# Optimization experiments

Measured on AMD Instinct MI355X. Metric: run time of the kernel, lower is better.

Reference implementation:

```python
import jax, jax.numpy as jnp
import numpy as np

F = 256       # in_src/in_dst feature dim (feat_dict)
HID = 256     # hidden_dim
K = 16        # sampled neighbors per dst node (fixed fan-out)
N_REVIEW = 16384
N_USER = 65536
N_PRODUCT = 65536
EPS = 1e-5


def setup_inputs() -> dict:
    key = jax.random.key(0)
    ks = jax.random.split(key, 24)
    rn = lambda k, shape, s=0.05: jax.random.normal(k, shape, jnp.float32) * s
    inp = {
        'x_user': jax.random.normal(ks[0], (N_USER, F), jnp.float32),
        'x_product': jax.random.normal(ks[1], (N_PRODUCT, F), jnp.float32),
        'x_review': jax.random.normal(ks[2], (N_REVIEW, F), jnp.float32),
        'nbr_user': jax.random.randint(ks[3], (N_REVIEW, K), 0, N_USER),
        'nbr_product': jax.random.randint(ks[4], (N_REVIEW, K), 0, N_PRODUCT),
    }
    i = 5
    for pre in ('u_', 'p_'):
        inp[pre + 'Wih'] = rn(ks[i], (4 * F, F)); i += 1      # LSTM input weights (gates i,f,g,o)
        inp[pre + 'Whh'] = rn(ks[i], (4 * F, F)); i += 1      # LSTM hidden weights
        inp[pre + 'bih'] = jnp.zeros((4 * F,), jnp.float32)
        inp[pre + 'bhh'] = jnp.zeros((4 * F,), jnp.float32)
        inp[pre + 'Wself'] = rn(ks[i], (HID, F)); i += 1      # SAGEConv fc_self
        inp[pre + 'Wneigh'] = rn(ks[i], (HID, F)); i += 1     # SAGEConv fc_neigh
        inp[pre + 'bconv'] = jnp.zeros((HID,), jnp.float32)   # SAGEConv bias
    inp['ln_g'] = jnp.ones((HID,), jnp.float32)
    inp['ln_b'] = jnp.zeros((HID,), jnp.float32)
    inp['bn_g'] = jnp.ones((HID,), jnp.float32)
    inp['bn_b'] = jnp.zeros((HID,), jnp.float32)
    inp['W1'] = rn(ks[i], (HID, HID)); i += 1
    inp['b1'] = jnp.zeros((HID,), jnp.float32)
    inp['W2'] = rn(ks[i], (2, HID)); i += 1
    inp['b2'] = jnp.zeros((2,), jnp.float32)
    return inp


def _lstm_last(x, Wih, Whh, bih, bhh):
    # x: [N, K, F] neighbor sequences; returns final hidden state [N, F]
    n, _, f = x.shape
    b = bih + bhh
    def step(carry, xt):  # xt: [N, F]
        h, c = carry
        gates = xt @ Wih.T + h @ Whh.T + b  # [N, 4F]
        ig, fg, gg, og = jnp.split(gates, 4, axis=-1)
        c = jax.nn.sigmoid(fg) * c + jax.nn.sigmoid(ig) * jnp.tanh(gg)
        h = jax.nn.sigmoid(og) * jnp.tanh(c)
        return (h, c), None
    h0 = jnp.zeros((n, f), x.dtype)
    (h, _), _ = jax.lax.scan(step, (h0, h0), jnp.swapaxes(x, 0, 1))
    return h


def _sage_rel(x_src, x_dst, nbr, Wih, Whh, bih, bhh, Wself, Wneigh, bconv):
    # gather neighbor features [N_dst, K, F] (feat_drop is identity at eval)
    nb = x_src[nbr]
    h_neigh = _lstm_last(nb, Wih, Whh, bih, bhh)            # [N_dst, F]
    rst = x_dst @ Wself.T + h_neigh @ Wneigh.T + bconv       # [N_dst, HID]
    return jax.nn.gelu(rst, approximate=False)               # activation=nn.GELU()


def reference(x_user, x_product, x_review, nbr_user, nbr_product,
              u_Wih, u_Whh, u_bih, u_bhh, u_Wself, u_Wneigh, u_bconv,
              p_Wih, p_Whh, p_bih, p_bhh, p_Wself, p_Wneigh, p_bconv,
              ln_g, ln_b, bn_g, bn_b, W1, b1, W2, b2):
    # HeteroGraphConv(aggregate='sum') over the two relations into 'review'
    h = (_sage_rel(x_user, x_review, nbr_user, u_Wih, u_Whh, u_bih, u_bhh,
                   u_Wself, u_Wneigh, u_bconv)
         + _sage_rel(x_product, x_review, nbr_product, p_Wih, p_Whh, p_bih, p_bhh,
                     p_Wself, p_Wneigh, p_bconv))
    # LayerNorm
    mu = jnp.mean(h, axis=-1, keepdims=True)
    var = jnp.var(h, axis=-1, keepdims=True)
    h = (h - mu) * jax.lax.rsqrt(var + EPS) * ln_g + ln_b
    # clf head: Dropout (identity at eval) -> BatchNorm1d (batch stats) -> MLP
    bm = jnp.mean(h, axis=0, keepdims=True)
    bv = jnp.var(h, axis=0, keepdims=True)
    h = (h - bm) * jax.lax.rsqrt(bv + EPS) * bn_g + bn_b
    h = jax.nn.gelu(h @ W1.T + b1, approximate=False)
    return h @ W2.T + b2  # [N_REVIEW, 2]
```

## Files before the change

kernel.cpp:

```cpp
#include <hip/hip_runtime.h>
#include <math.h>

#define NREV 16384
#define NUSER 65536
#define NPROD 65536
#define KNBR 16
#define LDK 72

typedef __attribute__((ext_vector_type(8))) short short8;
typedef __attribute__((ext_vector_type(4))) float f32x4;
typedef unsigned short u16;

__device__ __forceinline__ u16 f2bf(float f){
  union { float f; unsigned u; } x; x.f = f;
  unsigned r = x.u + 0x7fffu + ((x.u >> 16) & 1u);
  return (u16)(r >> 16);
}
__device__ __forceinline__ float bf2f(u16 u){
  union { unsigned u; float f; } x; x.u = ((unsigned)u) << 16;
  return x.f;
}
__device__ __forceinline__ float fexp2(float x){ return __builtin_amdgcn_exp2f(x); }
__device__ __forceinline__ float frcp(float x){ return __builtin_amdgcn_rcpf(x); }
#define LOG2E 1.4426950408889634f
__device__ __forceinline__ float sigf(float x){ return frcp(1.f + fexp2(-LOG2E*x)); }
__device__ __forceinline__ float tanh_fast(float x){ return 1.f - 2.f*frcp(1.f + fexp2(2.f*LOG2E*x)); }
__device__ __forceinline__ float gelu_fast(float x){
  float u = 0.7978845608f*x*(1.f + 0.044715f*x*x);
  return 0.5f*x*(1.f + tanh_fast(u));
}

__global__ void cvt_kernel(const float* __restrict__ src, u16* __restrict__ dst, int n4){
  int i = blockIdx.x*256 + threadIdx.x;
  if(i < n4){
    float4 v = reinterpret_cast<const float4*>(src)[i];
    ushort4 o; o.x=f2bf(v.x); o.y=f2bf(v.y); o.z=f2bf(v.z); o.w=f2bf(v.w);
    reinterpret_cast<ushort4*>(dst)[i] = o;
  }
}

__global__ void pack_lstm_kernel(const float* __restrict__ Wihp, const float* __restrict__ Whhp,
                                 const float* __restrict__ bihp, const float* __restrict__ bhhp,
                                 u16* __restrict__ Bpp, float* __restrict__ bpp){
  int n = blockIdx.x;
  int g = n & 3, j = n >> 2;
  int m = g*256 + j;
  int k = threadIdx.x;
  Bpp[(size_t)n*512 + k]       = f2bf(Wihp[(size_t)m*256 + k]);
  Bpp[(size_t)n*512 + 256 + k] = f2bf(Whhp[(size_t)m*256 + k]);
  if(k == 0) bpp[n] = bihp[m] + bhhp[m];
}

__global__ void pack_sage_kernel(const float* __restrict__ Wselfp, const float* __restrict__ Wneighp,
                                 u16* __restrict__ Bsp){
  int n = blockIdx.x;
  int k = threadIdx.x;
  Bsp[(size_t)n*512 + k]       = f2bf(Wselfp[(size_t)n*256 + k]);
  Bsp[(size_t)n*512 + 256 + k] = f2bf(Wneighp[(size_t)n*256 + k]);
}

__global__ __launch_bounds__(256, 4) void xw_kernel(
    const float* __restrict__ x, const u16* __restrict__ Bp,
    const float* __restrict__ bp, u16* __restrict__ xwout)
{
  __shared__ u16 sA[128*LDK];
  __shared__ u16 sB[128*LDK];
  int tid = threadIdx.x;
  int p = blockIdx.x;
  int xcd = p & 7, g = p >> 3;
  int nt = g & 7;
  int rt = (g >> 3) * 8 + xcd;
  f32x4 acc[4][4];
  #pragma unroll
  for(int i=0;i<4;++i)
    #pragma unroll
    for(int j=0;j<4;++j) acc[i][j] = (f32x4){0.f,0.f,0.f,0.f};
  int lane = tid & 63, w = tid >> 6, wr = w >> 1, wc = w & 1;
  int ci = tid & 7, r0 = tid >> 3;
  int rrow = lane & 15, lhi = lane >> 4, kb = lhi * 8;

  for(int kt=0; kt<4; ++kt){
    __syncthreads();
    #pragma unroll
    for(int pp=0; pp<4; ++pp){
      int row = pp*32 + r0;
      const float* srcA = x + (size_t)(rt*128 + row)*256 + kt*64 + ci*8;
      float4 a0 = *(const float4*)srcA;
      float4 a1 = *(const float4*)(srcA + 4);
      short8 s;
      s[0]=f2bf(a0.x); s[1]=f2bf(a0.y); s[2]=f2bf(a0.z); s[3]=f2bf(a0.w);
      s[4]=f2bf(a1.x); s[5]=f2bf(a1.y); s[6]=f2bf(a1.z); s[7]=f2bf(a1.w);
      *(short8*)&sA[row*LDK + ci*8] = s;
      *(short8*)&sB[row*LDK + ci*8] =
        *(const short8*)(Bp + (size_t)(nt*128 + row)*512 + kt*64 + ci*8);
    }
    __syncthreads();
    #pragma unroll
    for(int kk=0; kk<2; ++kk){
      short8 af[4], bfv[4];
      #pragma unroll
      for(int ni=0;ni<4;++ni) af[ni]  = *(const short8*)&sB[(wc*64+ni*16+rrow)*LDK + kk*32 + kb];
      #pragma unroll
      for(int mi=0;mi<4;++mi) bfv[mi] = *(const short8*)&sA[(wr*64+mi*16+rrow)*LDK + kk*32 + kb];
      #pragma unroll
      for(int ni=0;ni<4;++ni)
        #pragma unroll
        for(int mi=0;mi<4;++mi)
          acc[ni][mi] = __builtin_amdgcn_mfma_f32_16x16x32_bf16(af[ni], bfv[mi], acc[ni][mi], 0, 0, 0);
    }
  }
  #pragma unroll
  for(int mi=0;mi<4;++mi){
    size_t node = (size_t)(rt*128 + wr*64 + mi*16 + rrow);
    u16* dst = xwout + node*1024;
    #pragma unroll
    for(int ni=0;ni<4;++ni){
      int n0 = nt*128 + wc*64 + ni*16 + lhi*4;
      float4 bv = *(const float4*)&bp[n0];
      ushort4 o;
      o.x = f2bf(acc[ni][mi][0] + bv.x);
      o.y = f2bf(acc[ni][mi][1] + bv.y);
      o.z = f2bf(acc[ni][mi][2] + bv.z);
      o.w = f2bf(acc[ni][mi][3] + bv.w);
      *(ushort4*)(dst + n0) = o;
    }
  }
}

__global__ __launch_bounds__(256, 3) void lstm_step10_kernel(
    const u16* __restrict__ xw, const int* __restrict__ nbr, int t,
    const u16* __restrict__ Bh,
    const u16* __restrict__ hin, u16* __restrict__ hout, float* __restrict__ cT)
{
  __shared__ u16 sA[128*LDK];
  __shared__ u16 sB[128*LDK];
  int tid = threadIdx.x;
  int p = blockIdx.x;
  int xcd = p & 7, g = p >> 3;
  int nt = g & 7;
  int rt = (g >> 3) * 8 + xcd;
  int lane = tid & 63, w = tid >> 6, wr = w >> 1, wc = w & 1;
  int ci = tid & 7, r0 = tid >> 3;
  int rrow = lane & 15, lhi = lane >> 4, kb = lhi * 8;

  int node[4];
  #pragma unroll
  for(int mi=0;mi<4;++mi)
    node[mi] = nbr[(size_t)(rt*128 + wr*64 + mi*16 + rrow)*KNBR + t];
  ushort4 xv[4][4];
  #pragma unroll
  for(int mi=0;mi<4;++mi)
    #pragma unroll
    for(int ni=0;ni<4;++ni){
      int n0 = nt*128 + wc*64 + ni*16 + lhi*4;
      xv[mi][ni] = *(const ushort4*)(xw + (size_t)node[mi]*1024 + n0);
    }

  f32x4 acc[4][4];
  #pragma unroll
  for(int i=0;i<4;++i)
    #pragma unroll
    for(int j=0;j<4;++j) acc[i][j] = (f32x4){0.f,0.f,0.f,0.f};

  if(t > 0){
    for(int kt=0; kt<4; ++kt){
      __syncthreads();
      #pragma unroll
      for(int pp=0; pp<4; ++pp){
        int row = pp*32 + r0;
        *(short8*)&sA[row*LDK + ci*8] =
          *(const short8*)(hin + (size_t)(rt*128 + row)*256 + kt*64 + ci*8);
        *(short8*)&sB[row*LDK + ci*8] =
          *(const short8*)(Bh + (size_t)(nt*128 + row)*512 + kt*64 + ci*8);
      }
      __syncthreads();
      #pragma unroll
      for(int kk=0; kk<2; ++kk){
        short8 af[4], bfv[4];
        #pragma unroll
        for(int ni=0;ni<4;++ni) af[ni]  = *(const short8*)&sB[(wc*64+ni*16+rrow)*LDK + kk*32 + kb];
        #pragma unroll
        for(int mi=0;mi<4;++mi) bfv[mi] = *(const short8*)&sA[(wr*64+mi*16+rrow)*LDK + kk*32 + kb];
        #pragma unroll
        for(int ni=0;ni<4;++ni)
          #pragma unroll
          for(int mi=0;mi<4;++mi)
            acc[ni][mi] = __builtin_amdgcn_mfma_f32_16x16x32_bf16(af[ni], bfv[mi], acc[ni][mi], 0, 0, 0);
      }
    }
  }

  float cv[4][4];
  #pragma unroll
  for(int mi=0;mi<4;++mi)
    #pragma unroll
    for(int ni=0;ni<4;++ni){
      cv[mi][ni] = 0.f;
      if(t > 0){
        int j = nt*32 + wc*16 + ni*4 + lhi;
        cv[mi][ni] = cT[(size_t)j*NREV + rt*128 + wr*64 + mi*16 + rrow];
      }
    }

  #pragma unroll
  for(int mi=0;mi<4;++mi){
    int rg = rt*128 + wr*64 + mi*16 + rrow;
    #pragma unroll
    for(int ni=0;ni<4;++ni){
      int j = nt*32 + wc*16 + ni*4 + lhi;
      float ig = bf2f(xv[mi][ni].x) + acc[ni][mi][0];
      float fg = bf2f(xv[mi][ni].y) + acc[ni][mi][1];
      float gg = bf2f(xv[mi][ni].z) + acc[ni][mi][2];
      float og = bf2f(xv[mi][ni].w) + acc[ni][mi][3];
      float cn = sigf(fg)*cv[mi][ni] + sigf(ig)*tanh_fast(gg);
      cT[(size_t)j*NREV + rg] = cn;
      hout[(size_t)rg*256 + j] = f2bf(sigf(og)*tanh_fast(cn));
    }
  }
}

template<int MODE>
__global__ __launch_bounds__(256) void gemm_act_kernel(
    const u16* __restrict__ A0, const u16* __restrict__ A1,
    const u16* __restrict__ Bp, const float* __restrict__ bias,
    float* __restrict__ outF, u16* __restrict__ outH)
{
  constexpr int KT   = (MODE == 2) ? 4 : 8;
  constexpr int KTOT = KT * 64;
  __shared__ u16 sA[128*LDK];
  __shared__ u16 sB[128*LDK];
  int tid = threadIdx.x;
  int rt = blockIdx.x, nt = blockIdx.y;
  f32x4 acc[4][4];
  #pragma unroll
  for(int i=0;i<4;++i)
    #pragma unroll
    for(int j=0;j<4;++j) acc[i][j] = (f32x4){0.f,0.f,0.f,0.f};
  int lane = tid & 63, w = tid >> 6, wr = w >> 1, wc = w & 1;
  int ci = tid & 7, r0 = tid >> 3;
  int rrow = lane & 15, kb = (lane >> 4) * 8;

  for(int kt=0; kt<KT; ++kt){
    __syncthreads();
    #pragma unroll
    for(int pp=0; pp<4; ++pp){
      int row = pp*32 + r0;
      const u16* srcA = (kt < 4)
        ? (A0 + ((size_t)(rt*128 + row))*256 + kt*64)
        : (A1 + ((size_t)(rt*128 + row))*256 + (kt-4)*64);
      *(short8*)&sA[row*LDK + ci*8] = *(const short8*)(srcA + ci*8);
      const u16* srcB = Bp + ((size_t)(nt*128 + row))*KTOT + kt*64;
      *(short8*)&sB[row*LDK + ci*8] = *(const short8*)(srcB + ci*8);
    }
    __syncthreads();
    #pragma unroll
    for(int kk=0; kk<2; ++kk){
      short8 af[4], bfv[4];
      #pragma unroll
      for(int mi=0;mi<4;++mi) af[mi] = *(const short8*)&sA[(wr*64+mi*16+rrow)*LDK + kk*32 + kb];
      #pragma unroll
      for(int ni=0;ni<4;++ni) bfv[ni] = *(const short8*)&sB[(wc*64+ni*16+rrow)*LDK + kk*32 + kb];
      #pragma unroll
      for(int mi=0;mi<4;++mi)
        #pragma unroll
        for(int ni=0;ni<4;++ni)
          acc[mi][ni] = __builtin_amdgcn_mfma_f32_16x16x32_bf16(af[mi], bfv[ni], acc[mi][ni], 0, 0, 0);
    }
  }
  #pragma unroll
  for(int mi=0;mi<4;++mi)
    #pragma unroll
    for(int ni=0;ni<4;++ni){
      int col  = nt*128 + wc*64 + ni*16 + rrow;
      int rowb = rt*128 + wr*64 + mi*16 + (lane>>4)*4;
      float bv = bias[col];
      #pragma unroll
      for(int q=0;q<4;++q){
        float x = acc[mi][ni][q] + bv;
        float gl = gelu_fast(x);
        size_t idx = (size_t)(rowb+q)*256 + col;
        if(MODE == 0)      outF[idx] = gl;
        else if(MODE == 1) outF[idx] += gl;
        else               outH[idx] = f2bf(gl);
      }
    }
}

__global__ void ln_kernel(const float* __restrict__ hs, const float* __restrict__ g,
                          const float* __restrict__ b, u16* __restrict__ hlnp){
  int w = threadIdx.x >> 6, lane = threadIdx.x & 63;
  int r = blockIdx.x*4 + w;
  const float* row = hs + (size_t)r*256;
  float4 v = *(const float4*)(row + lane*4);
  float s  = v.x+v.y+v.z+v.w;
  float ss = v.x*v.x + v.y*v.y + v.z*v.z + v.w*v.w;
  #pragma unroll
  for(int d=1; d<64; d<<=1){ s += __shfl_xor(s, d, 64); ss += __shfl_xor(ss, d, 64); }
  float mu  = s  * (1.f/256.f);
  float var = ss * (1.f/256.f) - mu*mu;
  float rs  = rsqrtf(var + 1e-5f);
  float4 gv = *(const float4*)(g + lane*4);
  float4 bv = *(const float4*)(b + lane*4);
  ushort4 o;
  o.x = f2bf((v.x-mu)*rs*gv.x + bv.x);
  o.y = f2bf((v.y-mu)*rs*gv.y + bv.y);
  o.z = f2bf((v.z-mu)*rs*gv.z + bv.z);
  o.w = f2bf((v.w-mu)*rs*gv.w + bv.w);
  *(ushort4*)(hlnp + (size_t)r*256 + lane*4) = o;
}

__global__ void colstats_kernel(const u16* __restrict__ hlnp, float* __restrict__ cs, float* __restrict__ cq){
  int cix = threadIdx.x;
  size_t rb = (size_t)blockIdx.x * 128;
  float s=0.f, q=0.f;
  for(int rr=0; rr<128; ++rr){
    float v = bf2f(hlnp[(rb+rr)*256 + cix]);
    s += v; q += v*v;
  }
  atomicAdd(&cs[cix], s);
  atomicAdd(&cq[cix], q);
}

__global__ void bnstat_kernel(const float* __restrict__ cs, const float* __restrict__ cq,
                              const float* __restrict__ bng, const float* __restrict__ bnb,
                              float* __restrict__ bns, float* __restrict__ bnt){
  int cix = threadIdx.x;
  float bm = cs[cix] * (1.f/16384.f);
  float bv = cq[cix] * (1.f/16384.f) - bm*bm;
  float s  = bng[cix] * rsqrtf(bv + 1e-5f);
  bns[cix] = s;
  bnt[cix] = bnb[cix] - bm*s;
}

__global__ void w1fold_kernel(const float* __restrict__ W1p, const float* __restrict__ b1p,
                              const float* __restrict__ bns, const float* __restrict__ bnt,
                              u16* __restrict__ W1fp, float* __restrict__ b1fp){
  __shared__ float red[4];
  int n = blockIdx.x, k = threadIdx.x;
  int lane = k & 63, w = k >> 6;
  float wv = W1p[(size_t)n*256 + k];
  W1fp[(size_t)n*256 + k] = f2bf(wv * bns[k]);
  float p = wv * bnt[k];
  #pragma unroll
  for(int d=1; d<64; d<<=1) p += __shfl_xor(p, d, 64);
  if(lane == 0) red[w] = p;
  __syncthreads();
  if(k == 0) b1fp[n] = b1p[n] + red[0] + red[1] + red[2] + red[3];
}

__global__ void head_kernel(const u16* __restrict__ z, const float* __restrict__ W2p,
                            const float* __restrict__ b2p, float* __restrict__ outp){
  int w = threadIdx.x >> 6, lane = threadIdx.x & 63;
  int r = blockIdx.x*4 + w;
  const u16* zr = z + (size_t)r*256;
  ushort4 v = *(const ushort4*)(zr + lane*4);
  float z0=bf2f(v.x), z1v=bf2f(v.y), z2=bf2f(v.z), z3=bf2f(v.w);
  float4 wa = *(const float4*)(W2p + lane*4);
  float4 wb = *(const float4*)(W2p + 256 + lane*4);
  float p0 = z0*wa.x + z1v*wa.y + z2*wa.z + z3*wa.w;
  float p1 = z0*wb.x + z1v*wb.y + z2*wb.z + z3*wb.w;
  #pragma unroll
  for(int d=1; d<64; d<<=1){ p0 += __shfl_xor(p0,d,64); p1 += __shfl_xor(p1,d,64); }
  if(lane == 0){
    outp[(size_t)r*2]   = p0 + b2p[0];
    outp[(size_t)r*2+1] = p1 + b2p[1];
  }
}

extern "C" void kernel_launch(void* const* d_in, const int* in_sizes, int n_in,
                              void* d_out, int out_size, void* d_ws, size_t ws_size,
                              hipStream_t stream){
  (void)in_sizes; (void)n_in; (void)out_size;
  const float* x_user    = (const float*)d_in[0];
  const float* x_product = (const float*)d_in[1];
  const float* x_review  = (const float*)d_in[2];
  const int*   nbr_user  = (const int*)d_in[3];
  const int*   nbr_prod  = (const int*)d_in[4];
  const float* Wih[2]    = {(const float*)d_in[5],  (const float*)d_in[12]};
  const float* Whh[2]    = {(const float*)d_in[6],  (const float*)d_in[13]};
  const float* bih[2]    = {(const float*)d_in[7],  (const float*)d_in[14]};
  const float* bhh[2]    = {(const float*)d_in[8],  (const float*)d_in[15]};
  const float* Wself[2]  = {(const float*)d_in[9],  (const float*)d_in[16]};
  const float* Wneigh[2] = {(const float*)d_in[10], (const float*)d_in[17]};
  const float* bconv[2]  = {(const float*)d_in[11], (const float*)d_in[18]};
  const float* ln_g=(const float*)d_in[19], *ln_b=(const float*)d_in[20];
  const float* bn_g=(const float*)d_in[21], *bn_b=(const float*)d_in[22];
  const float* W1=(const float*)d_in[23], *b1=(const float*)d_in[24];
  const float* W2=(const float*)d_in[25], *b2=(const float*)d_in[26];
  float* out = (float*)d_out;

  char* base = (char*)d_ws;
  size_t off = 0;
  auto alloc = [&](size_t bytes)->char* { char* r = base + off; off += (bytes + 255) & ~(size_t)255; return r; };
  u16*   xr   = (u16*)  alloc((size_t)NREV*256*2);
  float* hsum = (float*)alloc((size_t)NREV*256*4);
  u16*   Bp[2]; Bp[0]=(u16*)alloc(1024*512*2); Bp[1]=(u16*)alloc(1024*512*2);
  float* bp[2]; bp[0]=(float*)alloc(4096);     bp[1]=(float*)alloc(4096);
  u16*   Bs[2]; Bs[0]=(u16*)alloc(256*512*2);  Bs[1]=(u16*)alloc(256*512*2);
  float* csum = (float*)alloc(1024);
  float* csq  = (float*)alloc(1024);
  float* bns  = (float*)alloc(1024);
  float* bnt  = (float*)alloc(1024);
  u16*   W1f  = (u16*)  alloc(256*256*2);
  float* b1f  = (float*)alloc(1024);
  u16*   hA   = (u16*)  alloc((size_t)NREV*256*2);
  u16*   hB   = (u16*)  alloc((size_t)NREV*256*2);
  float* cT   = (float*)alloc((size_t)NREV*256*4);
  u16*   xW   = (u16*)  alloc((size_t)NUSER*1024*2);
  if(off > ws_size) return;
  u16* hln = hA;
  u16* z1  = hB;

  cvt_kernel<<<dim3(4096),256,0,stream>>>(x_review, xr, NREV*256/4);
  for(int rel=0; rel<2; ++rel){
    pack_lstm_kernel<<<dim3(1024),256,0,stream>>>(Wih[rel],Whh[rel],bih[rel],bhh[rel],Bp[rel],bp[rel]);
    pack_sage_kernel<<<dim3(256), 256,0,stream>>>(Wself[rel],Wneigh[rel],Bs[rel]);
  }
  hipMemsetAsync(csum, 0, 1024, stream);
  hipMemsetAsync(csq,  0, 1024, stream);

  for(int rel=0; rel<2; ++rel){
    const float* xs = rel ? x_product : x_user;
    const int*   nb = rel ? nbr_prod  : nbr_user;
    xw_kernel<<<dim3(4096),256,0,stream>>>(xs, Bp[rel], bp[rel], xW);
    u16 *hin = hB, *hout = hA;
    for(int t=0; t<KNBR; ++t){
      lstm_step10_kernel<<<dim3(1024),256,0,stream>>>(xW, nb, t, Bp[rel] + 256, hin, hout, cT);
      u16* tmp = hin; hin = hout; hout = tmp;
    }
    if(rel == 0)
      gemm_act_kernel<0><<<dim3(128,2),256,0,stream>>>(xr, hin, Bs[0], bconv[0], hsum, nullptr);
    else
      gemm_act_kernel<1><<<dim3(128,2),256,0,stream>>>(xr, hin, Bs[1], bconv[1], hsum, nullptr);
  }

  ln_kernel<<<dim3(4096),256,0,stream>>>(hsum, ln_g, ln_b, hln);
  colstats_kernel<<<dim3(128),256,0,stream>>>(hln, csum, csq);
  bnstat_kernel<<<dim3(1),256,0,stream>>>(csum, csq, bn_g, bn_b, bns, bnt);
  w1fold_kernel<<<dim3(256),256,0,stream>>>(W1, b1, bns, bnt, W1f, b1f);
  gemm_act_kernel<2><<<dim3(128,2),256,0,stream>>>(hln, nullptr, W1f, b1f, nullptr, z1);
  head_kernel<<<dim3(4096),256,0,stream>>>(z1, W2, b2, out);
}
```

Before: 1.196 ms.

## Split LSTM step tile across 8 waves with 512-thread blocks

The per-timestep LSTM kernel now launches 512 threads per block instead of 256. Each of the 8 waves computes a 64x32 sub-tile rather than 64x64, which halves the per-wave accumulators, gathered xW values and cell-state registers. Cooperative shared-memory loading is remapped so each thread loads two 16-byte chunks from one row. The aim is more waves in flight to hide gather and global latency, at the cost of more A-fragment LDS reads per MFMA and heavier barrier synchronisation.

```diff
diff --git a/kernel.cpp b/kernel.cpp
--- a/kernel.cpp
+++ b/kernel.cpp
@@ -127,7 +127,7 @@
   }
 }
 
-__global__ __launch_bounds__(256, 3) void lstm_step10_kernel(
+__global__ __launch_bounds__(512, 2) void lstm_step11_kernel(
     const u16* __restrict__ xw, const int* __restrict__ nbr, int t,
     const u16* __restrict__ Bh,
     const u16* __restrict__ hin, u16* __restrict__ hout, float* __restrict__ cT)
@@ -139,26 +139,27 @@
   int xcd = p & 7, g = p >> 3;
   int nt = g & 7;
   int rt = (g >> 3) * 8 + xcd;
-  int lane = tid & 63, w = tid >> 6, wr = w >> 1, wc = w & 1;
-  int ci = tid & 7, r0 = tid >> 3;
+  int lane = tid & 63, w = tid >> 6;
+  int wrr = w & 1, wnn = w >> 1;
+  int ci2 = (tid & 3) * 2, r0 = tid >> 2;
   int rrow = lane & 15, lhi = lane >> 4, kb = lhi * 8;
 
   int node[4];
   #pragma unroll
   for(int mi=0;mi<4;++mi)
-    node[mi] = nbr[(size_t)(rt*128 + wr*64 + mi*16 + rrow)*KNBR + t];
-  ushort4 xv[4][4];
+    node[mi] = nbr[(size_t)(rt*128 + wrr*64 + mi*16 + rrow)*KNBR + t];
+  ushort4 xv[4][2];
   #pragma unroll
   for(int mi=0;mi<4;++mi)
     #pragma unroll
-    for(int ni=0;ni<4;++ni){
-      int n0 = nt*128 + wc*64 + ni*16 + lhi*4;
+    for(int ni=0;ni<2;++ni){
+      int n0 = nt*128 + wnn*32 + ni*16 + lhi*4;
       xv[mi][ni] = *(const ushort4*)(xw + (size_t)node[mi]*1024 + n0);
     }
 
-  f32x4 acc[4][4];
-  #pragma unroll
-  for(int i=0;i<4;++i)
+  f32x4 acc[2][4];
+  #pragma unroll
+  for(int i=0;i<2;++i)
     #pragma unroll
     for(int j=0;j<4;++j) acc[i][j] = (f32x4){0.f,0.f,0.f,0.f};
 
@@ -166,23 +167,22 @@
     for(int kt=0; kt<4; ++kt){
       __syncthreads();
       #pragma unroll
-      for(int pp=0; pp<4; ++pp){
-        int row = pp*32 + r0;
-        *(short8*)&sA[row*LDK + ci*8] =
-          *(const short8*)(hin + (size_t)(rt*128 + row)*256 + kt*64 + ci*8);
-        *(short8*)&sB[row*LDK + ci*8] =
-          *(const short8*)(Bh + (size_t)(nt*128 + row)*512 + kt*64 + ci*8);
+      for(int q=0;q<2;++q){
+        *(short8*)&sA[r0*LDK + (ci2+q)*8] =
+          *(const short8*)(hin + (size_t)(rt*128 + r0)*256 + kt*64 + (ci2+q)*8);
+        *(short8*)&sB[r0*LDK + (ci2+q)*8] =
+          *(const short8*)(Bh + (size_t)(nt*128 + r0)*512 + kt*64 + (ci2+q)*8);
       }
       __syncthreads();
       #pragma unroll
       for(int kk=0; kk<2; ++kk){
-        short8 af[4], bfv[4];
+        short8 af[2], bfv[4];
         #pragma unroll
-        for(int ni=0;ni<4;++ni) af[ni]  = *(const short8*)&sB[(wc*64+ni*16+rrow)*LDK + kk*32 + kb];
+        for(int ni=0;ni<2;++ni) af[ni]  = *(const short8*)&sB[(wnn*32+ni*16+rrow)*LDK + kk*32 + kb];
         #pragma unroll
-        for(int mi=0;mi<4;++mi) bfv[mi] = *(const short8*)&sA[(wr*64+mi*16+rrow)*LDK + kk*32 + kb];
+        for(int mi=0;mi<4;++mi) bfv[mi] = *(const short8*)&sA[(wrr*64+mi*16+rrow)*LDK + kk*32 + kb];
         #pragma unroll
-        for(int ni=0;ni<4;++ni)
+        for(int ni=0;ni<2;++ni)
           #pragma unroll
           for(int mi=0;mi<4;++mi)
             acc[ni][mi] = __builtin_amdgcn_mfma_f32_16x16x32_bf16(af[ni], bfv[mi], acc[ni][mi], 0, 0, 0);
@@ -190,24 +190,24 @@
     }
   }
 
-  float cv[4][4];
+  float cv[4][2];
   #pragma unroll
   for(int mi=0;mi<4;++mi)
     #pragma unroll
-    for(int ni=0;ni<4;++ni){
+    for(int ni=0;ni<2;++ni){
       cv[mi][ni] = 0.f;
       if(t > 0){
-        int j = nt*32 + wc*16 + ni*4 + lhi;
-        cv[mi][ni] = cT[(size_t)j*NREV + rt*128 + wr*64 + mi*16 + rrow];
+        int j = nt*32 + wnn*8 + ni*4 + lhi;
+        cv[mi][ni] = cT[(size_t)j*NREV + rt*128 + wrr*64 + mi*16 + rrow];
       }
     }
 
   #pragma unroll
   for(int mi=0;mi<4;++mi){
-    int rg = rt*128 + wr*64 + mi*16 + rrow;
-    #pragma unroll
-    for(int ni=0;ni<4;++ni){
-      int j = nt*32 + wc*16 + ni*4 + lhi;
+    int rg = rt*128 + wrr*64 + mi*16 + rrow;
+    #pragma unroll
+    for(int ni=0;ni<2;++ni){
+      int j = nt*32 + wnn*8 + ni*4 + lhi;
       float ig = bf2f(xv[mi][ni].x) + acc[ni][mi][0];
       float fg = bf2f(xv[mi][ni].y) + acc[ni][mi][1];
       float gg = bf2f(xv[mi][ni].z) + acc[ni][mi][2];
@@ -425,7 +425,7 @@
     xw_kernel<<<dim3(4096),256,0,stream>>>(xs, Bp[rel], bp[rel], xW);
     u16 *hin = hB, *hout = hA;
     for(int t=0; t<KNBR; ++t){
-      lstm_step10_kernel<<<dim3(1024),256,0,stream>>>(xW, nb, t, Bp[rel] + 256, hin, hout, cT);
+      lstm_step11_kernel<<<dim3(1024),512,0,stream>>>(xW, nb, t, Bp[rel] + 256, hin, hout, cT);
       u16* tmp = hin; hin = hout; hout = tmp;
     }
     if(rel == 0)
```

New measurement: 1.227 ms. 2.6% more time.
